# Kernel optimization log

Hardware: AMD Instinct MI355X
Metric: run time of the kernel (lower is better)

The kernel has to match this reference:

```python
import jax, jax.numpy as jnp
import numpy as np
from jax import lax

B, H, W, C = 8, 96, 96, 256
N_HEADS = 8
HEAD_DIM = C // N_HEADS
KS = 5  # depthwise LePE kernel


def setup_inputs() -> dict:
    key = jax.random.key(0)
    ks = jax.random.split(key, 12)
    s = 0.05  # xavier-ish scale for weights
    return {
        "x": jax.random.normal(ks[0], (B, H, W, C), jnp.float32),
        "encoder_layer": jax.random.normal(ks[1], (B, H, W, C), jnp.float32),
        "Wq": jax.random.normal(ks[2], (C, C), jnp.float32) * s,
        "bq": jnp.zeros((C,), jnp.float32),
        "Wk": jax.random.normal(ks[3], (C, C), jnp.float32) * s,
        "bk": jnp.zeros((C,), jnp.float32),
        "Wv": jax.random.normal(ks[4], (C, C), jnp.float32) * s,
        "bv": jnp.zeros((C,), jnp.float32),
        "conv_w": jax.random.normal(ks[5], (KS, KS, 1, C), jnp.float32) * s,  # HWIO depthwise
        "conv_b": jnp.zeros((C,), jnp.float32),
        "Wo": jax.random.normal(ks[6], (C, C), jnp.float32) * s,
        "bo": jnp.zeros((C,), jnp.float32),
        "rel_pos": jnp.zeros((1,), jnp.int32),  # unused by the module
    }


def _dwconv(v, conv_w, conv_b):
    # depthwise 5x5, stride 1, pad 2, NHWC
    y = lax.conv_general_dilated(
        v, conv_w, window_strides=(1, 1), padding=((2, 2), (2, 2)),
        dimension_numbers=("NHWC", "HWIO", "NHWC"), feature_group_count=v.shape[-1])
    return y + conv_b


def reference(x, encoder_layer, Wq, bq, Wk, bk, Wv, bv, conv_w, conv_b, Wo, bo, rel_pos):
    b, h, w, c = x.shape
    n, d = N_HEADS, c // N_HEADS
    scaling = jnp.asarray(d, x.dtype) ** -0.5

    q = x @ Wq + bq
    k = x @ Wk + bk + encoder_layer  # embed_dim != 64 branch
    v = x @ Wv + bv + encoder_layer

    lepe = _dwconv(v, conv_w, conv_b)  # (b,h,w,c)
    k = k * scaling

    qr = q.reshape(b, h, w, n, d)
    kr = k.reshape(b, h, w, n, d)
    vr = v.reshape(b, h, w, n, d)

    # width-wise axial attention: scores (b,h,n,w,w), LOG-softmax over keys
    A_w = jax.nn.log_softmax(jnp.einsum("bhind,bhjnd->bhnij", qr, kr), axis=-1)
    v1 = jnp.einsum("bhnij,bhjnd->bhind", A_w, vr)  # (b,h,w,n,d)

    # height-wise axial attention: scores (b,w,n,h,h), LOG-softmax over keys
    A_h = jax.nn.log_softmax(jnp.einsum("biwnd,bjwnd->bwnij", qr, kr), axis=-1)
    out = jnp.einsum("bwnij,bjwnd->biwnd", A_h, v1)  # (b,h,w,n,d)

    out = out.reshape(b, h, w, c) + lepe
    return out @ Wo + bo
```

## Files before the change

kernel.cpp:

```cpp
#include <hip/hip_runtime.h>

#define B_ 8
#define S_ 96
#define C_ 256
#define NH_ 8
#define D_ 32
#define M_ (B_*S_*S_)
static const size_t SZ = (size_t)M_ * C_;

typedef unsigned short u16;
typedef short bf16x8 __attribute__((ext_vector_type(8)));
typedef _Float16 hf8 __attribute__((ext_vector_type(8)));
typedef float f32x4 __attribute__((ext_vector_type(4)));

__device__ __forceinline__ u16 f2b(float f) {
    unsigned u = __float_as_uint(f);
    return (u16)((u + 0x7FFFu + ((u >> 16) & 1u)) >> 16);
}
__device__ __forceinline__ float b2f(u16 h) { return __uint_as_float(((unsigned)h) << 16); }
__device__ __forceinline__ u16 f2h(float f) {
    _Float16 h = (_Float16)f;
    return __builtin_bit_cast(u16, h);
}

__device__ __forceinline__ void gload16(const u16* g, u16* l) {
    __builtin_amdgcn_global_load_lds(
        (const __attribute__((address_space(1))) u16*)g,
        (__attribute__((address_space(3))) u16*)l, 16, 0, 0);
}

__global__ __launch_bounds__(256) void prep_x(
    const float* __restrict__ x, u16* __restrict__ xb)
{
    size_t base = ((size_t)blockIdx.x * 256 + threadIdx.x) * 8;
    float4 a = *(const float4*)(x + base);
    float4 b = *(const float4*)(x + base + 4);
    u16 o[8] = { f2b(a.x), f2b(a.y), f2b(a.z), f2b(a.w),
                 f2b(b.x), f2b(b.y), f2b(b.z), f2b(b.w) };
    *(int4*)(xb + base) = *(int4*)o;
}

__global__ __launch_bounds__(256) void prep_w(
    const float* __restrict__ Wq, const float* __restrict__ Wk,
    const float* __restrict__ Wv, const float* __restrict__ Wo,
    u16* __restrict__ WT)
{
    int id = blockIdx.x * 256 + threadIdx.x;
    int w = id >> 16;
    int r = id & 65535;
    int n = r >> 8;
    int kk = r & 255;
    const float* Wp = (w == 0) ? Wq : (w == 1) ? Wk : (w == 2) ? Wv : Wo;
    WT[(size_t)id] = f2b(Wp[(size_t)kk * 256 + n]);
}

__global__ __launch_bounds__(256) void prep_cw(
    const float* __restrict__ cw, u16* __restrict__ cwh)
{
    int id = blockIdx.x * 256 + threadIdx.x;
    cwh[id] = f2h(cw[id]);
}

#define STG(lds, gbase, k0)                                                     \
    _Pragma("unroll")                                                           \
    for (int i_ = 0; i_ < 2; ++i_) {                                            \
        int r16 = wave * 32 + i_ * 16;                                          \
        gload16((gbase) + (size_t)(r16 + lrow) * C_ + (k0) + slot * 8,          \
                (lds) + r16 * 32);                                              \
    }

__global__ __launch_bounds__(256, 3) void proj_q(
    const u16* __restrict__ xb, const u16* __restrict__ WT,
    const float* __restrict__ bq, u16* __restrict__ q)
{
    __shared__ u16 sA[2 * 4096];
    __shared__ u16 sB[2 * 4096];
    const int t = threadIdx.x;
    const int colbase = blockIdx.x * 128;
    const int m0 = blockIdx.y * 128;
    const int wave = t >> 6, lane = t & 63;
    const int wr = wave >> 1, wc = wave & 1;
    const int l16 = lane & 15, kg = lane >> 4;
    const int lrow = lane >> 2, slot = lane & 3;

    const u16* gA = xb + (size_t)m0 * C_;
    const u16* gB = WT + (size_t)colbase * C_;

    f32x4 acc[4][4];
#pragma unroll
    for (int i = 0; i < 4; ++i)
#pragma unroll
        for (int j = 0; j < 4; ++j) acc[i][j] = (f32x4){0.f, 0.f, 0.f, 0.f};

    STG(sA, gA, 0); STG(sB, gB, 0);
    __syncthreads();
#pragma unroll
    for (int it = 0; it < 8; ++it) {
        const int cur = it & 1;
        if (it < 7) { STG(sA + (cur ^ 1) * 4096, gA, (it + 1) * 32);
                      STG(sB + (cur ^ 1) * 4096, gB, (it + 1) * 32); }
        bf16x8 af[4], bf[4];
#pragma unroll
        for (int mi = 0; mi < 4; ++mi)
            af[mi] = *(const bf16x8*)(sA + cur * 4096 + (wr * 64 + mi * 16 + l16) * 32 + kg * 8);
#pragma unroll
        for (int ni = 0; ni < 4; ++ni)
            bf[ni] = *(const bf16x8*)(sB + cur * 4096 + (wc * 64 + ni * 16 + l16) * 32 + kg * 8);
#pragma unroll
        for (int mi = 0; mi < 4; ++mi)
#pragma unroll
            for (int ni = 0; ni < 4; ++ni)
                acc[mi][ni] = __builtin_amdgcn_mfma_f32_16x16x32_bf16(
                    af[mi], bf[ni], acc[mi][ni], 0, 0, 0);
        if (it < 7) __syncthreads();
    }

#pragma unroll
    for (int mi = 0; mi < 4; ++mi)
#pragma unroll
        for (int ni = 0; ni < 4; ++ni) {
            int col = colbase + wc * 64 + ni * 16 + l16;
            float bqv = bq[col];
#pragma unroll
            for (int r = 0; r < 4; ++r) {
                int row = m0 + wr * 64 + mi * 16 + kg * 4 + r;
                q[(size_t)row * 256 + col] = f2b(acc[mi][ni][r] + bqv);
            }
        }
}

__global__ __launch_bounds__(256, 2) void proj_kv(
    const u16* __restrict__ xb, const float* __restrict__ enc,
    const u16* __restrict__ WT,
    const float* __restrict__ bk, const float* __restrict__ bv,
    u16* __restrict__ k, u16* __restrict__ v)
{
    __shared__ u16 sA[2 * 4096];
    __shared__ u16 sB0[2 * 4096];
    __shared__ u16 sB1[2 * 4096];
    const int t = threadIdx.x;
    const int colbase = blockIdx.x * 128;
    const int m0 = blockIdx.y * 128;
    const int wave = t >> 6, lane = t & 63;
    const int wr = wave >> 1, wc = wave & 1;
    const int l16 = lane & 15, kg = lane >> 4;
    const int lrow = lane >> 2, slot = lane & 3;

    const u16* gA = xb + (size_t)m0 * C_;
    const u16* gB0 = WT + 65536 + (size_t)colbase * C_;
    const u16* gB1 = WT + 2 * 65536 + (size_t)colbase * C_;

    f32x4 acck[4][4], accv[4][4];
#pragma unroll
    for (int i = 0; i < 4; ++i)
#pragma unroll
        for (int j = 0; j < 4; ++j) {
            acck[i][j] = (f32x4){0.f, 0.f, 0.f, 0.f};
            accv[i][j] = (f32x4){0.f, 0.f, 0.f, 0.f};
        }

    STG(sA, gA, 0); STG(sB0, gB0, 0); STG(sB1, gB1, 0);
    __syncthreads();
#pragma unroll
    for (int it = 0; it < 8; ++it) {
        const int cur = it & 1;
        if (it < 7) { STG(sA + (cur ^ 1) * 4096, gA, (it + 1) * 32);
                      STG(sB0 + (cur ^ 1) * 4096, gB0, (it + 1) * 32);
                      STG(sB1 + (cur ^ 1) * 4096, gB1, (it + 1) * 32); }
        bf16x8 af[4], b0[4], b1[4];
#pragma unroll
        for (int mi = 0; mi < 4; ++mi)
            af[mi] = *(const bf16x8*)(sA + cur * 4096 + (wr * 64 + mi * 16 + l16) * 32 + kg * 8);
#pragma unroll
        for (int ni = 0; ni < 4; ++ni) {
            b0[ni] = *(const bf16x8*)(sB0 + cur * 4096 + (wc * 64 + ni * 16 + l16) * 32 + kg * 8);
            b1[ni] = *(const bf16x8*)(sB1 + cur * 4096 + (wc * 64 + ni * 16 + l16) * 32 + kg * 8);
        }
#pragma unroll
        for (int mi = 0; mi < 4; ++mi)
#pragma unroll
            for (int ni = 0; ni < 4; ++ni) {
                acck[mi][ni] = __builtin_amdgcn_mfma_f32_16x16x32_bf16(
                    af[mi], b0[ni], acck[mi][ni], 0, 0, 0);
                accv[mi][ni] = __builtin_amdgcn_mfma_f32_16x16x32_bf16(
                    af[mi], b1[ni], accv[mi][ni], 0, 0, 0);
            }
        if (it < 7) __syncthreads();
    }

    const float SCALE = 0.17677669529663687f;
#pragma unroll
    for (int mi = 0; mi < 4; ++mi)
#pragma unroll
        for (int ni = 0; ni < 4; ++ni) {
            int col = colbase + wc * 64 + ni * 16 + l16;
            float bkv = bk[col], bvv = bv[col];
#pragma unroll
            for (int r = 0; r < 4; ++r) {
                int row = m0 + wr * 64 + mi * 16 + kg * 4 + r;
                size_t off = (size_t)row * 256 + col;
                float e = enc[off];
                k[off] = f2b((acck[mi][ni][r] + bkv + e) * SCALE);
                v[off] = f2h(accv[mi][ni][r] + bvv + e);
            }
        }
}

__global__ __launch_bounds__(256) void dwconv5x5(
    const u16* __restrict__ vh, const u16* __restrict__ cwh,
    const float* __restrict__ cb, u16* __restrict__ lepeb)
{
    size_t tid = (size_t)blockIdx.x * 256 + threadIdx.x;
    int c8 = (int)(tid & 31);
    size_t rest = tid >> 5;
    int wi = (int)(rest % 24);
    size_t tmp = rest / 24;
    int h = (int)(tmp % S_);
    int b = (int)(tmp / S_);
    int w0 = wi * 4;
    int c0 = c8 * 8;

    hf8 z;
#pragma unroll
    for (int q = 0; q < 8; ++q) z[q] = (_Float16)0.f;
    hf8 acc[4] = { z, z, z, z };

#pragma unroll
    for (int dy = -2; dy <= 2; ++dy) {
        int hy = h + dy;
        if (hy < 0 || hy >= S_) continue;
        const u16* rowp = vh + (((size_t)b * S_ + hy) * S_) * C_ + c0;
        hf8 vr[8];
#pragma unroll
        for (int i = 0; i < 8; ++i) {
            int c = w0 - 2 + i;
            vr[i] = (c >= 0 && c < S_) ? *(const hf8*)(rowp + (size_t)c * C_) : z;
        }
#pragma unroll
        for (int dx = 0; dx < 5; ++dx) {
            hf8 ww = *(const hf8*)(cwh + (size_t)((dy + 2) * 5 + dx) * C_ + c0);
#pragma unroll
            for (int r = 0; r < 4; ++r) acc[r] += vr[dx + r] * ww;
        }
    }

    float4 cb0 = *(const float4*)(cb + c0);
    float4 cb1 = *(const float4*)(cb + c0 + 4);
    float cbv[8] = { cb0.x, cb0.y, cb0.z, cb0.w, cb1.x, cb1.y, cb1.z, cb1.w };
    size_t pix0 = ((size_t)b * S_ + h) * S_ + w0;
#pragma unroll
    for (int r = 0; r < 4; ++r) {
        u16 o[8];
#pragma unroll
        for (int q = 0; q < 8; ++q) o[q] = f2b((float)acc[r][q] + cbv[q]);
        *(int4*)(lepeb + (pix0 + r) * C_ + c0) = *(int4*)o;
    }
}

template<int HM>
__global__ __launch_bounds__(128, 3) void axial(
    const u16* __restrict__ qb, const u16* __restrict__ kb,
    const void* __restrict__ vin, void* __restrict__ vout,
    const u16* __restrict__ lep, int ofac, int pstride)
{
    __shared__ u16 sQ[96][56];
    __shared__ u16 sK[96][56];
    __shared__ u16 sVT[HM + 1][32][104];
    __shared__ u16 sAh[2][16][40];
    __shared__ u16 sAl[2][16][40];

    const int t = threadIdx.x;
    const int wave = t >> 6, lane = t & 63;
    const int l16 = lane & 15, kg = lane >> 4;

    const int n = blockIdx.x & 7;
    const int o = (blockIdx.x >> 3) % 96;
    const int b = blockIdx.x / (8 * 96);
    const size_t base = ((size_t)b * 9216 + (size_t)o * ofac) * C_ + n * D_;

    if (t < 96) {
        const u16* gq = qb + base + (size_t)t * pstride;
        const u16* gk = kb + base + (size_t)t * pstride;
#pragma unroll
        for (int c = 0; c < 4; ++c) {
            *(int4*)&sQ[t][c * 8] = *(const int4*)(gq + c * 8);
            *(int4*)&sK[t][c * 8] = *(const int4*)(gk + c * 8);
        }
    }
    if (HM == 0) {
        const u16* vb = (const u16*)vin;
#pragma unroll
        for (int p = 0; p < 3; ++p) {
            int j = p * 32 + (t >> 2);
            int dc = (t & 3) * 8;
            int4 raw = *(const int4*)(vb + base + (size_t)j * pstride + dc);
            const u16* e = (const u16*)&raw;
#pragma unroll
            for (int q = 0; q < 8; ++q) sVT[0][dc + q][j] = e[q];
        }
    } else {
        const float* v1 = (const float*)vin;
#pragma unroll
        for (int p = 0; p < 6; ++p) {
            int j = p * 16 + (t >> 3);
            int db = (t & 7) * 4;
            float4 f = *(const float4*)(v1 + base + (size_t)j * pstride + db);
            float fv[4] = { f.x, f.y, f.z, f.w };
#pragma unroll
            for (int q = 0; q < 4; ++q) {
                u16 hi = f2b(fv[q]);
                sVT[0][db + q][j] = hi;
                sVT[HM][db + q][j] = f2b(fv[q] - b2f(hi));
            }
        }
    }
    __syncthreads();

    bf16x8 kf[6];
#pragma unroll
    for (int f = 0; f < 6; ++f)
        kf[f] = *(const bf16x8*)&sK[f * 16 + l16][kg * 8];

    const f32x4 zero = {0.f, 0.f, 0.f, 0.f};

    for (int p = 0; p < 3; ++p) {
        const int g = wave * 3 + p;
        bf16x8 qf = *(const bf16x8*)&sQ[g * 16 + l16][kg * 8];
        f32x4 s[6];
#pragma unroll
        for (int f = 0; f < 6; ++f)
            s[f] = __builtin_amdgcn_mfma_f32_16x16x32_bf16(kf[f], qf, zero, 0, 0, 0);

        float m = s[0][0];
#pragma unroll
        for (int f = 0; f < 6; ++f)
#pragma unroll
            for (int r = 0; r < 4; ++r) m = fmaxf(m, s[f][r]);
        m = fmaxf(m, __shfl_xor(m, 16));
        m = fmaxf(m, __shfl_xor(m, 32));
        float l = 0.f;
#pragma unroll
        for (int f = 0; f < 6; ++f)
#pragma unroll
            for (int r = 0; r < 4; ++r) l += __expf(s[f][r] - m);
        l += __shfl_xor(l, 16);
        l += __shfl_xor(l, 32);
        float lse = m + __logf(l);

        u16 ah[6][4], al[6][4];
#pragma unroll
        for (int f = 0; f < 6; ++f)
#pragma unroll
            for (int r = 0; r < 4; ++r) {
                float a = s[f][r] - lse;
                ah[f][r] = (HM == 0) ? f2h(a) : f2b(a);
                if (HM) al[f][r] = f2b(a - b2f(ah[f][r]));
            }

        f32x4 pacc[2] = { zero, zero };
#pragma unroll
        for (int c = 0; c < 3; ++c) {
#pragma unroll
            for (int fi = 0; fi < 2; ++fi)
#pragma unroll
                for (int r = 0; r < 4; ++r) {
                    int col = fi * 16 + kg * 4 + r;
                    sAh[wave][l16][col] = ah[2 * c + fi][r];
                    if (HM) sAl[wave][l16][col] = al[2 * c + fi][r];
                }
            if (HM == 0) {
                hf8 ahf = *(const hf8*)&sAh[wave][l16][kg * 8];
#pragma unroll
                for (int nf = 0; nf < 2; ++nf) {
                    hf8 vt = *(const hf8*)&sVT[0][nf * 16 + l16][c * 32 + kg * 8];
                    pacc[nf] = __builtin_amdgcn_mfma_f32_16x16x32_f16(ahf, vt, pacc[nf], 0, 0, 0);
                }
            } else {
                bf16x8 ahf = *(const bf16x8*)&sAh[wave][l16][kg * 8];
                bf16x8 alf = *(const bf16x8*)&sAl[wave][l16][kg * 8];
#pragma unroll
                for (int nf = 0; nf < 2; ++nf) {
                    bf16x8 vt = *(const bf16x8*)&sVT[0][nf * 16 + l16][c * 32 + kg * 8];
                    bf16x8 vtl = *(const bf16x8*)&sVT[HM][nf * 16 + l16][c * 32 + kg * 8];
                    pacc[nf] = __builtin_amdgcn_mfma_f32_16x16x32_bf16(ahf, vt, pacc[nf], 0, 0, 0);
                    pacc[nf] = __builtin_amdgcn_mfma_f32_16x16x32_bf16(ahf, vtl, pacc[nf], 0, 0, 0);
                    pacc[nf] = __builtin_amdgcn_mfma_f32_16x16x32_bf16(alf, vt, pacc[nf], 0, 0, 0);
                }
            }
        }

#pragma unroll
        for (int nf = 0; nf < 2; ++nf)
#pragma unroll
            for (int r = 0; r < 4; ++r) {
                int qi = g * 16 + kg * 4 + r;
                size_t off = base + (size_t)qi * pstride + nf * 16 + l16;
                if (HM == 0) {
                    ((float*)vout)[off] = pacc[nf][r];
                } else {
                    float lv = b2f(lep[off]);
                    ((u16*)vout)[off] = f2b(pacc[nf][r] + lv);
                }
            }
    }
}

__global__ __launch_bounds__(256, 3) void out_gemm(
    const u16* __restrict__ o2b, const u16* __restrict__ WoT,
    const float* __restrict__ bo, float* __restrict__ out)
{
    __shared__ u16 sA[2 * 4096];
    __shared__ u16 sB[2 * 4096];
    const int t = threadIdx.x;
    const int colbase = blockIdx.x * 128;
    const int m0 = blockIdx.y * 128;
    const int wave = t >> 6, lane = t & 63;
    const int wr = wave >> 1, wc = wave & 1;
    const int l16 = lane & 15, kg = lane >> 4;
    const int lrow = lane >> 2, slot = lane & 3;

    const u16* gA = o2b + (size_t)m0 * C_;
    const u16* gB = WoT + (size_t)colbase * C_;

    f32x4 acc[4][4];
#pragma unroll
    for (int i = 0; i < 4; ++i)
#pragma unroll
        for (int j = 0; j < 4; ++j) acc[i][j] = (f32x4){0.f, 0.f, 0.f, 0.f};

    STG(sA, gA, 0); STG(sB, gB, 0);
    __syncthreads();
#pragma unroll
    for (int it = 0; it < 8; ++it) {
        const int cur = it & 1;
        if (it < 7) { STG(sA + (cur ^ 1) * 4096, gA, (it + 1) * 32);
                      STG(sB + (cur ^ 1) * 4096, gB, (it + 1) * 32); }
        bf16x8 af[4], bf[4];
#pragma unroll
        for (int mi = 0; mi < 4; ++mi)
            af[mi] = *(const bf16x8*)(sA + cur * 4096 + (wr * 64 + mi * 16 + l16) * 32 + kg * 8);
#pragma unroll
        for (int ni = 0; ni < 4; ++ni)
            bf[ni] = *(const bf16x8*)(sB + cur * 4096 + (wc * 64 + ni * 16 + l16) * 32 + kg * 8);
#pragma unroll
        for (int mi = 0; mi < 4; ++mi)
#pragma unroll
            for (int ni = 0; ni < 4; ++ni)
                acc[mi][ni] = __builtin_amdgcn_mfma_f32_16x16x32_bf16(
                    af[mi], bf[ni], acc[mi][ni], 0, 0, 0);
        if (it < 7) __syncthreads();
    }

#pragma unroll
    for (int mi = 0; mi < 4; ++mi)
#pragma unroll
        for (int ni = 0; ni < 4; ++ni) {
            int col = colbase + wc * 64 + ni * 16 + l16;
            float bv_ = bo[col];
#pragma unroll
            for (int r = 0; r < 4; ++r) {
                int row = m0 + wr * 64 + mi * 16 + kg * 4 + r;
                out[(size_t)row * 256 + col] = acc[mi][ni][r] + bv_;
            }
        }
}

extern "C" void kernel_launch(void* const* d_in, const int* in_sizes, int n_in,
                              void* d_out, int out_size, void* d_ws, size_t ws_size,
                              hipStream_t stream)
{
    const float* x   = (const float*)d_in[0];
    const float* enc = (const float*)d_in[1];
    const float* Wq  = (const float*)d_in[2];
    const float* bq  = (const float*)d_in[3];
    const float* Wk  = (const float*)d_in[4];
    const float* bk  = (const float*)d_in[5];
    const float* Wv  = (const float*)d_in[6];
    const float* bv  = (const float*)d_in[7];
    const float* cw  = (const float*)d_in[8];
    const float* cb  = (const float*)d_in[9];
    const float* Wo  = (const float*)d_in[10];
    const float* bo  = (const float*)d_in[11];

    u16* qbuf = (u16*)d_ws;
    u16* kbuf = qbuf + SZ;
    u16* vbuf = kbuf + SZ;
    u16* WT   = vbuf + SZ;
    u16* cwh  = WT + 4 * 65536;
    u16* xb   = cwh + 6400;
    u16* lep  = xb + SZ;
    float* v1 = (float*)d_out;

    prep_x<<<9216, 256, 0, stream>>>(x, xb);
    prep_w<<<1024, 256, 0, stream>>>(Wq, Wk, Wv, Wo, WT);
    prep_cw<<<25, 256, 0, stream>>>(cw, cwh);
    proj_q<<<dim3(2, 576), 256, 0, stream>>>(xb, WT, bq, qbuf);
    proj_kv<<<dim3(2, 576), 256, 0, stream>>>(xb, enc, WT, bk, bv, kbuf, vbuf);
    dwconv5x5<<<2304, 256, 0, stream>>>(vbuf, cwh, cb, lep);
    axial<0><<<B_ * 96 * NH_, 128, 0, stream>>>(qbuf, kbuf, vbuf, v1, nullptr, 96, 256);
    axial<1><<<B_ * 96 * NH_, 128, 0, stream>>>(qbuf, kbuf, v1, qbuf, lep, 1, 96 * 256);
    out_gemm<<<dim3(2, 576), 256, 0, stream>>>(qbuf, WT + 3 * 65536, bo, (float*)d_out);
}
```

Measured before the change: 288.8 us.

## Merge Q/K/V projections into one GEMM kernel and swizzle LDS tiles

Replaces the separate proj_q and proj_kv kernels with a single proj_all kernel whose grid selects Q, K or V by blockIdx.x, so each block carries one accumulator set and uses less LDS. Adds an XOR swizzle on the LDS staging slot and on fragment reads to reduce bank conflicts in both the projection and output GEMMs. Raises the launch-bounds occupancy hint from 3 or 2 to 4. The trade-off is that the x tile is now loaded once per projection instead of being shared by K and V.

Result: slower. 368.6 us (+27.6%).

```diff
diff --git a/kernel.cpp b/kernel.cpp
--- a/kernel.cpp
+++ b/kernel.cpp
@@ -65,26 +65,33 @@
     _Pragma("unroll")                                                           \
     for (int i_ = 0; i_ < 2; ++i_) {                                            \
         int r16 = wave * 32 + i_ * 16;                                          \
-        gload16((gbase) + (size_t)(r16 + lrow) * C_ + (k0) + slot * 8,          \
+        gload16((gbase) + (size_t)(r16 + srow) * C_ + (k0) + sslot * 8,         \
                 (lds) + r16 * 32);                                              \
     }
-
-__global__ __launch_bounds__(256, 3) void proj_q(
-    const u16* __restrict__ xb, const u16* __restrict__ WT,
-    const float* __restrict__ bq, u16* __restrict__ q)
+#define FRAG(lds, cur, rowi) \
+    (*(const bf16x8*)((lds) + (cur) * 4096 + (rowi) * 32 + (kg ^ (((rowi) >> 1) & 3)) * 8))
+
+__global__ __launch_bounds__(256, 4) void proj_all(
+    const u16* __restrict__ xb, const float* __restrict__ enc,
+    const u16* __restrict__ WT,
+    const float* __restrict__ bq, const float* __restrict__ bk,
+    const float* __restrict__ bv,
+    u16* __restrict__ q, u16* __restrict__ k, u16* __restrict__ v)
 {
     __shared__ u16 sA[2 * 4096];
     __shared__ u16 sB[2 * 4096];
     const int t = threadIdx.x;
-    const int colbase = blockIdx.x * 128;
+    const int which = blockIdx.x >> 1;
+    const int colbase = (blockIdx.x & 1) * 128;
     const int m0 = blockIdx.y * 128;
     const int wave = t >> 6, lane = t & 63;
     const int wr = wave >> 1, wc = wave & 1;
     const int l16 = lane & 15, kg = lane >> 4;
-    const int lrow = lane >> 2, slot = lane & 3;
+    const int srow = lane >> 2;
+    const int sslot = (lane & 3) ^ ((lane >> 3) & 3);
 
     const u16* gA = xb + (size_t)m0 * C_;
-    const u16* gB = WT + (size_t)colbase * C_;
+    const u16* gB = WT + (size_t)which * 65536 + (size_t)colbase * C_;
 
     f32x4 acc[4][4];
 #pragma unroll
@@ -102,10 +109,10 @@
         bf16x8 af[4], bf[4];
 #pragma unroll
         for (int mi = 0; mi < 4; ++mi)
-            af[mi] = *(const bf16x8*)(sA + cur * 4096 + (wr * 64 + mi * 16 + l16) * 32 + kg * 8);
+            af[mi] = FRAG(sA, cur, wr * 64 + mi * 16 + l16);
 #pragma unroll
         for (int ni = 0; ni < 4; ++ni)
-            bf[ni] = *(const bf16x8*)(sB + cur * 4096 + (wc * 64 + ni * 16 + l16) * 32 + kg * 8);
+            bf[ni] = FRAG(sB, cur, wc * 64 + ni * 16 + l16);
 #pragma unroll
         for (int mi = 0; mi < 4; ++mi)
 #pragma unroll
@@ -115,93 +122,22 @@
         if (it < 7) __syncthreads();
     }
 
+    const float SCALE = 0.17677669529663687f;
+    const float* __restrict__ bias = (which == 0) ? bq : (which == 1) ? bk : bv;
 #pragma unroll
     for (int mi = 0; mi < 4; ++mi)
 #pragma unroll
         for (int ni = 0; ni < 4; ++ni) {
             int col = colbase + wc * 64 + ni * 16 + l16;
-            float bqv = bq[col];
-#pragma unroll
-            for (int r = 0; r < 4; ++r) {
-                int row = m0 + wr * 64 + mi * 16 + kg * 4 + r;
-                q[(size_t)row * 256 + col] = f2b(acc[mi][ni][r] + bqv);
-            }
-        }
-}
-
-__global__ __launch_bounds__(256, 2) void proj_kv(
-    const u16* __restrict__ xb, const float* __restrict__ enc,
-    const u16* __restrict__ WT,
-    const float* __restrict__ bk, const float* __restrict__ bv,
-    u16* __restrict__ k, u16* __restrict__ v)
-{
-    __shared__ u16 sA[2 * 4096];
-    __shared__ u16 sB0[2 * 4096];
-    __shared__ u16 sB1[2 * 4096];
-    const int t = threadIdx.x;
-    const int colbase = blockIdx.x * 128;
-    const int m0 = blockIdx.y * 128;
-    const int wave = t >> 6, lane = t & 63;
-    const int wr = wave >> 1, wc = wave & 1;
-    const int l16 = lane & 15, kg = lane >> 4;
-    const int lrow = lane >> 2, slot = lane & 3;
-
-    const u16* gA = xb + (size_t)m0 * C_;
-    const u16* gB0 = WT + 65536 + (size_t)colbase * C_;
-    const u16* gB1 = WT + 2 * 65536 + (size_t)colbase * C_;
-
-    f32x4 acck[4][4], accv[4][4];
-#pragma unroll
-    for (int i = 0; i < 4; ++i)
-#pragma unroll
-        for (int j = 0; j < 4; ++j) {
-            acck[i][j] = (f32x4){0.f, 0.f, 0.f, 0.f};
-            accv[i][j] = (f32x4){0.f, 0.f, 0.f, 0.f};
-        }
-
-    STG(sA, gA, 0); STG(sB0, gB0, 0); STG(sB1, gB1, 0);
-    __syncthreads();
-#pragma unroll
-    for (int it = 0; it < 8; ++it) {
-        const int cur = it & 1;
-        if (it < 7) { STG(sA + (cur ^ 1) * 4096, gA, (it + 1) * 32);
-                      STG(sB0 + (cur ^ 1) * 4096, gB0, (it + 1) * 32);
-                      STG(sB1 + (cur ^ 1) * 4096, gB1, (it + 1) * 32); }
-        bf16x8 af[4], b0[4], b1[4];
-#pragma unroll
-        for (int mi = 0; mi < 4; ++mi)
-            af[mi] = *(const bf16x8*)(sA + cur * 4096 + (wr * 64 + mi * 16 + l16) * 32 + kg * 8);
-#pragma unroll
-        for (int ni = 0; ni < 4; ++ni) {
-            b0[ni] = *(const bf16x8*)(sB0 + cur * 4096 + (wc * 64 + ni * 16 + l16) * 32 + kg * 8);
-            b1[ni] = *(const bf16x8*)(sB1 + cur * 4096 + (wc * 64 + ni * 16 + l16) * 32 + kg * 8);
-        }
-#pragma unroll
-        for (int mi = 0; mi < 4; ++mi)
-#pragma unroll
-            for (int ni = 0; ni < 4; ++ni) {
-                acck[mi][ni] = __builtin_amdgcn_mfma_f32_16x16x32_bf16(
-                    af[mi], b0[ni], acck[mi][ni], 0, 0, 0);
-                accv[mi][ni] = __builtin_amdgcn_mfma_f32_16x16x32_bf16(
-                    af[mi], b1[ni], accv[mi][ni], 0, 0, 0);
-            }
-        if (it < 7) __syncthreads();
-    }
-
-    const float SCALE = 0.17677669529663687f;
-#pragma unroll
-    for (int mi = 0; mi < 4; ++mi)
-#pragma unroll
-        for (int ni = 0; ni < 4; ++ni) {
-            int col = colbase + wc * 64 + ni * 16 + l16;
-            float bkv = bk[col], bvv = bv[col];
+            float bb = bias[col];
 #pragma unroll
             for (int r = 0; r < 4; ++r) {
                 int row = m0 + wr * 64 + mi * 16 + kg * 4 + r;
                 size_t off = (size_t)row * 256 + col;
-                float e = enc[off];
-                k[off] = f2b((acck[mi][ni][r] + bkv + e) * SCALE);
-                v[off] = f2h(accv[mi][ni][r] + bvv + e);
+                float cv = acc[mi][ni][r] + bb;
+                if (which == 0)      q[off] = f2b(cv);
+                else if (which == 1) k[off] = f2b((cv + enc[off]) * SCALE);
+                else                 v[off] = f2h(cv + enc[off]);
             }
         }
 }
@@ -405,7 +341,7 @@
     }
 }
 
-__global__ __launch_bounds__(256, 3) void out_gemm(
+__global__ __launch_bounds__(256, 4) void out_gemm(
     const u16* __restrict__ o2b, const u16* __restrict__ WoT,
     const float* __restrict__ bo, float* __restrict__ out)
 {
@@ -417,7 +353,8 @@
     const int wave = t >> 6, lane = t & 63;
     const int wr = wave >> 1, wc = wave & 1;
     const int l16 = lane & 15, kg = lane >> 4;
-    const int lrow = lane >> 2, slot = lane & 3;
+    const int srow = lane >> 2;
+    const int sslot = (lane & 3) ^ ((lane >> 3) & 3);
 
     const u16* gA = o2b + (size_t)m0 * C_;
     const u16* gB = WoT + (size_t)colbase * C_;
@@ -438,10 +375,10 @@
         bf16x8 af[4], bf[4];
 #pragma unroll
         for (int mi = 0; mi < 4; ++mi)
-            af[mi] = *(const bf16x8*)(sA + cur * 4096 + (wr * 64 + mi * 16 + l16) * 32 + kg * 8);
+            af[mi] = FRAG(sA, cur, wr * 64 + mi * 16 + l16);
 #pragma unroll
         for (int ni = 0; ni < 4; ++ni)
-            bf[ni] = *(const bf16x8*)(sB + cur * 4096 + (wc * 64 + ni * 16 + l16) * 32 + kg * 8);
+            bf[ni] = FRAG(sB, cur, wc * 64 + ni * 16 + l16);
 #pragma unroll
         for (int mi = 0; mi < 4; ++mi)
 #pragma unroll
@@ -494,8 +431,7 @@
     prep_x<<<9216, 256, 0, stream>>>(x, xb);
     prep_w<<<1024, 256, 0, stream>>>(Wq, Wk, Wv, Wo, WT);
     prep_cw<<<25, 256, 0, stream>>>(cw, cwh);
-    proj_q<<<dim3(2, 576), 256, 0, stream>>>(xb, WT, bq, qbuf);
-    proj_kv<<<dim3(2, 576), 256, 0, stream>>>(xb, enc, WT, bk, bv, kbuf, vbuf);
+    proj_all<<<dim3(6, 576), 256, 0, stream>>>(xb, enc, WT, bq, bk, bv, qbuf, kbuf, vbuf);
     dwconv5x5<<<2304, 256, 0, stream>>>(vbuf, cwh, cb, lep);
     axial<0><<<B_ * 96 * NH_, 128, 0, stream>>>(qbuf, kbuf, vbuf, v1, nullptr, 96, 256);
     axial<1><<<B_ * 96 * NH_, 128, 0, stream>>>(qbuf, kbuf, v1, qbuf, lep, 1, 96 * 256);
```
